# Optimization experiments

Hardware: AMD Instinct MI355X
Metric: run time of the kernel (lower is better)

Reference implementation:

```python
import jax, jax.numpy as jnp
import numpy as np

EMB = 768
HEADS = 12
HEAD_DIM = EMB // HEADS
# Source computes scores / scale with scale = head_dim**-0.5, i.e. scores * sqrt(head_dim)
INV_SCALE = float(HEAD_DIM) ** 0.5


def setup_inputs() -> dict:
    key = jax.random.key(0)
    k1, k2, k3, k4 = jax.random.split(key, 4)
    x = jax.random.normal(k1, (1, 4096, EMB), dtype=jnp.float32)
    qkv_w = jax.random.normal(k2, (3 * EMB, EMB), dtype=jnp.float32) * (EMB ** -0.5)
    out_w = jax.random.normal(k3, (EMB, EMB), dtype=jnp.float32) * (EMB ** -0.5)
    out_b = jax.random.normal(k4, (EMB,), dtype=jnp.float32) * 0.02
    return {"x": x, "qkv_w": qkv_w, "out_w": out_w, "out_b": out_b}


def reference(x, qkv_w, out_w, out_b):
    b, l, d = x.shape
    # qkv: torch Linear (no bias): x @ W^T -> [b, l, 3*d]
    qkv = jnp.einsum('bld,ed->ble', x, qkv_w)
    # rearrange 'b l (n h hd) -> n b h l hd'
    qkv = qkv.reshape(b, l, 3, HEADS, HEAD_DIM).transpose(2, 0, 3, 1, 4)
    q, k, v = qkv[0], qkv[1], qkv[2]
    # scores = (Q K^T) / scale, scale = head_dim**-0.5 => multiply by sqrt(head_dim)
    scores = jnp.einsum('bhqo,bhko->bhqk', q, k) * INV_SCALE
    attn = jax.nn.softmax(scores, axis=-1)  # [b, h, l, l]
    ctx = jnp.einsum('bhqk,bhko->bhqo', attn, v)  # [b, h, l, hd]
    ctx = ctx.transpose(0, 2, 1, 3).reshape(b, l, d)  # 'b h l hd -> b l (h hd)'
    out = jnp.einsum('bld,ed->ble', ctx, out_w) + out_b
    return out
```

## Files before the change

### kernel.cpp

```cpp
#include <hip/hip_runtime.h>

typedef __attribute__((ext_vector_type(8))) short short8;
typedef __attribute__((ext_vector_type(4))) float f32x4;

#define EMB 768
#define SEQ 4096
#define NH 12
#define HD 64
#define QSCALE 11.541560327111707f

#define GLOBAL_AS __attribute__((address_space(1)))
#define LDS_AS __attribute__((address_space(3)))

__device__ inline ushort f2bf(float v) {
  union { float f; unsigned int u; } x; x.f = v;
  unsigned int r = x.u + 0x7fffu + ((x.u >> 16) & 1u);
  return (ushort)(r >> 16);
}
__device__ inline float bf2f(ushort u) {
  union { float f; unsigned int u32; } x; x.u32 = ((unsigned int)u) << 16;
  return x.f;
}

__device__ inline float dpp_max16(float v) {
  int t;
  t = __builtin_amdgcn_update_dpp(0, __float_as_int(v), 0xB1, 0xf, 0xf, true);
  v = fmaxf(v, __int_as_float(t));
  t = __builtin_amdgcn_update_dpp(0, __float_as_int(v), 0x4E, 0xf, 0xf, true);
  v = fmaxf(v, __int_as_float(t));
  t = __builtin_amdgcn_update_dpp(0, __float_as_int(v), 0x124, 0xf, 0xf, true);
  v = fmaxf(v, __int_as_float(t));
  t = __builtin_amdgcn_update_dpp(0, __float_as_int(v), 0x128, 0xf, 0xf, true);
  v = fmaxf(v, __int_as_float(t));
  return v;
}

__global__ void split_all(const float* __restrict__ x, const float* __restrict__ qw,
                          const float* __restrict__ ow,
                          ushort* __restrict__ xh, ushort* __restrict__ xl,
                          ushort* __restrict__ qwh, ushort* __restrict__ qwl,
                          ushort* __restrict__ owh, int n14, int n24) {
  int i = blockIdx.x * blockDim.x + threadIdx.x;
  const float4* src;
  ushort4 *dh, *dl;
  int j;
  if (i < n14) {
    src = (const float4*)x; dh = (ushort4*)xh; dl = (ushort4*)xl; j = i;
  } else if (i < n14 + n24) {
    src = (const float4*)qw; dh = (ushort4*)qwh; dl = (ushort4*)qwl; j = i - n14;
  } else {
    j = i - n14 - n24;
    float4 v = ((const float4*)ow)[j];
    ushort4 h = {f2bf(v.x), f2bf(v.y), f2bf(v.z), f2bf(v.w)};
    ((ushort4*)owh)[j] = h;
    return;
  }
  float4 v = src[j];
  ushort4 h = {f2bf(v.x), f2bf(v.y), f2bf(v.z), f2bf(v.w)};
  ushort4 l = {f2bf(v.x - bf2f(h.x)), f2bf(v.y - bf2f(h.y)),
               f2bf(v.z - bf2f(h.z)), f2bf(v.w - bf2f(h.w))};
  dh[j] = h;
  dl[j] = l;
}

__global__ __launch_bounds__(256, 2) void gemm_bt_split(
    const ushort* __restrict__ Ah, const ushort* __restrict__ Al,
    const ushort* __restrict__ Bh, const ushort* __restrict__ Bl,
    int M, int N, int K, int mode,
    float* __restrict__ Cout, const float* __restrict__ bias,
    ushort* __restrict__ Qh, ushort* __restrict__ Ql,
    ushort* __restrict__ Kh, ushort* __restrict__ Kl,
    ushort* __restrict__ Vt) {
  __shared__ ushort smem[2][4 * 128 * 32];

  const int tid = threadIdx.x;
  const int lane = tid & 63;
  const int w = tid >> 6;
  const int wm = w >> 1, wn = w & 1;
  const int col = lane & 15, quad = lane >> 4;
  const int bm = blockIdx.x, bn = blockIdx.y;

  const bool oneterm = (mode == 2) || (mode == 1 && bn >= 12);
  const bool skipdma = oneterm && (w == 1 || w == 3);

  const ushort* gsrc = (w == 0)   ? Ah + (size_t)bm * 128 * K
                       : (w == 1) ? Al + (size_t)bm * 128 * K
                       : (w == 2) ? Bh + (size_t)bn * 128 * K
                                  : Bl + (size_t)bn * 128 * K;
  const int loff = w * 4096;
  const ushort* g0 = gsrc + (size_t)(lane >> 2) * K + (lane & 3) * 8;

  f32x4 acc[4][4];
  const f32x4 zz = {0.f, 0.f, 0.f, 0.f};
#pragma unroll
  for (int i = 0; i < 4; ++i)
#pragma unroll
    for (int j = 0; j < 4; ++j) acc[i][j] = zz;

#define GSTAGE(b, kt)                                                       \
  if (!skipdma) {                                                           \
    _Pragma("unroll") for (int i = 0; i < 8; ++i) {                         \
      __builtin_amdgcn_global_load_lds(                                     \
          (const GLOBAL_AS unsigned int*)(g0 + (size_t)i * 16 * K + (kt)),  \
          (LDS_AS unsigned int*)(&smem[b][loff + i * 512]), 16, 0, 0);      \
    }                                                                       \
  }

  GSTAGE(0, 0);
  const int nk = K / 32;
  for (int it = 0; it < nk; ++it) {
    const int buf = it & 1;
    asm volatile("s_waitcnt vmcnt(0)" ::: "memory");
    __syncthreads();
    if (it + 1 < nk) GSTAGE(buf ^ 1, (it + 1) * 32);

    const ushort* sAh = &smem[buf][0];
    const ushort* sAl = &smem[buf][4096];
    const ushort* sBh = &smem[buf][8192];
    const ushort* sBl = &smem[buf][12288];

    if (oneterm) {
      short8 fah[4], fbh[4];
#pragma unroll
      for (int t = 0; t < 4; ++t) {
        fah[t] = *(const short8*)(&sAh[(wm * 64 + t * 16 + col) * 32 + quad * 8]);
        fbh[t] = *(const short8*)(&sBh[(wn * 64 + t * 16 + col) * 32 + quad * 8]);
      }
#pragma unroll
      for (int tm = 0; tm < 4; ++tm)
#pragma unroll
        for (int tn = 0; tn < 4; ++tn)
          acc[tm][tn] = __builtin_amdgcn_mfma_f32_16x16x32_bf16(fah[tm], fbh[tn], acc[tm][tn], 0, 0, 0);
    } else {
      short8 fah[4], fal[4], fbh[4], fbl[4];
#pragma unroll
      for (int t = 0; t < 4; ++t) {
        int ra = (wm * 64 + t * 16 + col) * 32 + quad * 8;
        fah[t] = *(const short8*)(&sAh[ra]);
        fal[t] = *(const short8*)(&sAl[ra]);
        int rb = (wn * 64 + t * 16 + col) * 32 + quad * 8;
        fbh[t] = *(const short8*)(&sBh[rb]);
        fbl[t] = *(const short8*)(&sBl[rb]);
      }
#pragma unroll
      for (int tm = 0; tm < 4; ++tm)
#pragma unroll
        for (int tn = 0; tn < 4; ++tn) {
          acc[tm][tn] = __builtin_amdgcn_mfma_f32_16x16x32_bf16(fah[tm], fbh[tn], acc[tm][tn], 0, 0, 0);
          acc[tm][tn] = __builtin_amdgcn_mfma_f32_16x16x32_bf16(fah[tm], fbl[tn], acc[tm][tn], 0, 0, 0);
          acc[tm][tn] = __builtin_amdgcn_mfma_f32_16x16x32_bf16(fal[tm], fbh[tn], acc[tm][tn], 0, 0, 0);
        }
    }
  }

  const int m_base = bm * 128 + wm * 64;
  const int n_base = bn * 128 + wn * 64;

  if (mode != 1) {
#pragma unroll
    for (int tm = 0; tm < 4; ++tm)
#pragma unroll
      for (int tn = 0; tn < 4; ++tn) {
        int gn = n_base + tn * 16 + col;
        float b = bias[gn];
#pragma unroll
        for (int rr = 0; rr < 4; ++rr) {
          int gm = m_base + tm * 16 + quad * 4 + rr;
          Cout[(size_t)gm * N + gn] = acc[tm][tn][rr] + b;
        }
      }
  } else {
    int reg = bn / 6;
    if (reg < 2) {
#pragma unroll
      for (int tm = 0; tm < 4; ++tm)
#pragma unroll
        for (int tn = 0; tn < 4; ++tn) {
          int el = (bn % 6) * 128 + wn * 64 + tn * 16 + col;
          int hh = el >> 6, dd = el & 63;
#pragma unroll
          for (int rr = 0; rr < 4; ++rr) {
            int gm = m_base + tm * 16 + quad * 4 + rr;
            float v = acc[tm][tn][rr];
            if (reg == 0) {
              v *= QSCALE;
              ushort hi = f2bf(v);
              size_t idx = ((size_t)hh * SEQ + gm) * HD + dd;
              Qh[idx] = hi;
              Ql[idx] = f2bf(v - bf2f(hi));
            } else {
              ushort hi = f2bf(v);
              int pc = ((dd >> 3) ^ (gm & 7)) & 7;
              size_t idx = ((size_t)hh * SEQ + gm) * HD + pc * 8 + (dd & 7);
              Kh[idx] = hi;
              Kl[idx] = f2bf(v - bf2f(hi));
            }
          }
        }
    } else {
      __syncthreads();
      ushort* vt_tile = &smem[0][0];
#pragma unroll
      for (int tm = 0; tm < 4; ++tm)
#pragma unroll
        for (int tn = 0; tn < 4; ++tn) {
          int el = wn * 64 + tn * 16 + col;
#pragma unroll
          for (int rr = 0; rr < 4; ++rr) {
            int seq = wm * 64 + tm * 16 + quad * 4 + rr;
            int cc = (((seq >> 3) & 7) ^ (el & 7)) & 7;
            vt_tile[el * 128 + (seq & 64) + cc * 8 + (seq & 7)] = f2bf(acc[tm][tn][rr]);
          }
        }
      __syncthreads();
      int el = tid >> 1;
      int elg = (bn % 6) * 128 + el;
      int hh = elg >> 6, dd = elg & 63;
      ushort* grow = Vt + (size_t)(hh * HD + dd) * SEQ + bm * 128;
#pragma unroll
      for (int i = 0; i < 8; ++i) {
        int c = ((tid & 1) * 8 + i + el) & 15;
        *(uint4*)(grow + c * 8) = *(const uint4*)(&vt_tile[el * 128 + c * 8]);
      }
    }
  }
}

__global__ __launch_bounds__(256, 3) void attn_k(
    const ushort* __restrict__ Qh, const ushort* __restrict__ Ql,
    const ushort* __restrict__ Kh, const ushort* __restrict__ Kl,
    const ushort* __restrict__ Vt, ushort* __restrict__ Ch) {
  __shared__ ushort sKh[2][64 * 64];
  __shared__ ushort sKl[2][64 * 64];
  __shared__ ushort sVt[2][64 * 64];
  __shared__ ushort sP[4][16 * 32];

  const int tid = threadIdx.x, lane = tid & 63, w = tid >> 6;
  const int col = lane & 15, quad = lane >> 4;
  const int h = blockIdx.y;
  const int q0 = blockIdx.x * 64 + w * 16;

  const ushort* qh_base = Qh + ((size_t)h * SEQ + q0 + col) * HD;
  const ushort* ql_base = Ql + ((size_t)h * SEQ + q0 + col) * HD;
  short8 fqh[2], fql[2];
#pragma unroll
  for (int ks = 0; ks < 2; ++ks) {
    fqh[ks] = *(const short8*)(qh_base + ks * 32 + quad * 8);
    fql[ks] = *(const short8*)(ql_base + ks * 32 + quad * 8);
  }

  const short ONE = (short)0x3F80;
  const short8 ones = {ONE, ONE, ONE, ONE, ONE, ONE, ONE, ONE};

  float m2[4], ell[4];
  f32x4 o[4];
  const f32x4 zz = {0.f, 0.f, 0.f, 0.f};
#pragma unroll
  for (int i = 0; i < 4; ++i) { m2[i] = -1e30f; ell[i] = 0.f; o[i] = zz; }

  const ushort* khg = Kh + (size_t)h * SEQ * HD;
  const ushort* klg = Kl + (size_t)h * SEQ * HD;
  const ushort* vtg = Vt + (size_t)h * HD * SEQ;
  ushort* pw = &sP[w][0];

  const ushort* gp[6];
  ushort* lp[6];
  int gstep[6];
#pragma unroll
  for (int i = 0; i < 6; ++i) {
    int idx = w * 6 + i;
    int arr = idx >> 3, j = idx & 7;
    if (arr == 0) {
      gp[i] = khg + (size_t)(j * 8 + (lane >> 3)) * 64 + (lane & 7) * 8;
      lp[i] = &sKh[0][j * 512];
      gstep[i] = 64 * 64;
    } else if (arr == 1) {
      gp[i] = klg + (size_t)(j * 8 + (lane >> 3)) * 64 + (lane & 7) * 8;
      lp[i] = &sKl[0][j * 512];
      gstep[i] = 64 * 64;
    } else {
      gp[i] = vtg + (size_t)(j * 8 + (lane >> 3)) * SEQ + (lane & 7) * 8;
      lp[i] = &sVt[0][j * 512];
      gstep[i] = 64;
    }
  }

#pragma unroll
  for (int i = 0; i < 6; ++i) {
    __builtin_amdgcn_global_load_lds((const GLOBAL_AS unsigned int*)gp[i],
                                     (LDS_AS unsigned int*)lp[i], 16, 0, 0);
    gp[i] += gstep[i];
  }

  const int koff0 = (col * 64 + ((quad ^ (col & 7)) & 7) * 8) * 2;
  const int koff1 = (col * 64 + (((4 + quad) ^ (col & 7)) & 7) * 8) * 2;
  const int fpoff = (col * 32 + ((quad ^ (col & 3) ^ ((col >> 2) & 3)) & 3) * 8) * 2;
  const int voff0 = koff0;
  const int voff1 = koff1;

  auto do_iter = [&](int buf) {
    asm volatile("s_waitcnt vmcnt(0)" ::: "memory");
    __syncthreads();
#pragma unroll
    for (int i = 0; i < 6; ++i) {
      __builtin_amdgcn_global_load_lds(
          (const GLOBAL_AS unsigned int*)gp[i],
          (LDS_AS unsigned int*)(lp[i] + (buf ^ 1) * 4096), 16, 0, 0);
      gp[i] += gstep[i];
    }
    const char* kh = (const char*)&sKh[buf][0];
    const char* kl = (const char*)&sKl[buf][0];
    const char* vt = (const char*)&sVt[buf][0];

    f32x4 s[4];
#pragma unroll
    for (int tn = 0; tn < 4; ++tn) {
      f32x4 a = zz;
      short8 kh0 = *(const short8*)(kh + tn * 2048 + koff0);
      short8 kl0 = *(const short8*)(kl + tn * 2048 + koff0);
      short8 kh1 = *(const short8*)(kh + tn * 2048 + koff1);
      short8 kl1 = *(const short8*)(kl + tn * 2048 + koff1);
      a = __builtin_amdgcn_mfma_f32_16x16x32_bf16(fqh[0], kh0, a, 0, 0, 0);
      a = __builtin_amdgcn_mfma_f32_16x16x32_bf16(fqh[0], kl0, a, 0, 0, 0);
      a = __builtin_amdgcn_mfma_f32_16x16x32_bf16(fql[0], kh0, a, 0, 0, 0);
      a = __builtin_amdgcn_mfma_f32_16x16x32_bf16(fqh[1], kh1, a, 0, 0, 0);
      a = __builtin_amdgcn_mfma_f32_16x16x32_bf16(fqh[1], kl1, a, 0, 0, 0);
      a = __builtin_amdgcn_mfma_f32_16x16x32_bf16(fql[1], kh1, a, 0, 0, 0);
      s[tn] = a;
    }

    float lm[4];
#pragma unroll
    for (int rr = 0; rr < 4; ++rr)
      lm[rr] = fmaxf(fmaxf(s[0][rr], s[1][rr]), fmaxf(s[2][rr], s[3][rr]));
    int cond = (lm[0] <= m2[0]) && (lm[1] <= m2[1]) &&
               (lm[2] <= m2[2]) && (lm[3] <= m2[3]);
    if (!__all(cond)) {
      float alpha[4];
#pragma unroll
      for (int rr = 0; rr < 4; ++rr) {
        float vm = dpp_max16(lm[rr]);
        float mn = fmaxf(m2[rr], vm + 48.0f);
        alpha[rr] = exp2f(m2[rr] - mn);
        m2[rr] = mn;
        ell[rr] *= alpha[rr];
      }
#pragma unroll
      for (int td = 0; td < 4; ++td)
#pragma unroll
        for (int rr = 0; rr < 4; ++rr) o[td][rr] *= alpha[rr];
    }

    f32x4 psum = zz;
#pragma unroll
    for (int hh = 0; hh < 2; ++hh) {
#pragma unroll
      for (int t2 = 0; t2 < 2; ++t2) {
        int tn = hh * 2 + t2;
#pragma unroll
        for (int rr = 0; rr < 4; ++rr) {
          float p = exp2f(s[tn][rr] - m2[rr]);
          int row = quad * 4 + rr;
          int cc = t2 * 16 + col;
          int slot = ((cc >> 3) ^ rr ^ quad) & 3;
          pw[row * 32 + slot * 8 + (cc & 7)] =
              (ushort)(__float_as_uint(p) >> 16);
        }
      }
      asm volatile("s_waitcnt lgkmcnt(0)" ::: "memory");
      short8 fp = *(const short8*)((const char*)pw + fpoff);
      psum = __builtin_amdgcn_mfma_f32_16x16x32_bf16(fp, ones, psum, 0, 0, 0);
      const int vo = hh ? voff1 : voff0;
#pragma unroll
      for (int td = 0; td < 4; ++td) {
        short8 fv = *(const short8*)(vt + td * 2048 + vo);
        o[td] = __builtin_amdgcn_mfma_f32_16x16x32_bf16(fp, fv, o[td], 0, 0, 0);
      }
    }
#pragma unroll
    for (int rr = 0; rr < 4; ++rr) ell[rr] += psum[rr];
  };

  for (int kb = 0; kb < SEQ; kb += 128) {
    do_iter(0);
    do_iter(1);
  }

#pragma unroll
  for (int td = 0; td < 4; ++td)
#pragma unroll
    for (int rr = 0; rr < 4; ++rr) {
      float v = o[td][rr] / ell[rr];
      int l = q0 + quad * 4 + rr;
      int d = h * 64 + td * 16 + col;
      Ch[(size_t)l * EMB + d] = f2bf(v);
    }
}

extern "C" void kernel_launch(void* const* d_in, const int* in_sizes, int n_in,
                              void* d_out, int out_size, void* d_ws, size_t ws_size,
                              hipStream_t stream) {
  const float* x = (const float*)d_in[0];
  const float* qkv_w = (const float*)d_in[1];
  const float* out_w = (const float*)d_in[2];
  const float* out_b = (const float*)d_in[3];
  float* out = (float*)d_out;

  char* p = (char*)d_ws;
  auto carve = [&](size_t bytes) {
    char* q = p;
    p += (bytes + 255) & ~(size_t)255;
    return q;
  };
  const size_t NX = (size_t)SEQ * EMB;
  const size_t NQW = (size_t)3 * EMB * EMB;
  const size_t NOW = (size_t)EMB * EMB;
  const size_t NQKV = (size_t)NH * SEQ * HD;

  ushort* xh = (ushort*)carve(NX * 2);
  ushort* xl = (ushort*)carve(NX * 2);
  ushort* qwh = (ushort*)carve(NQW * 2);
  ushort* qwl = (ushort*)carve(NQW * 2);
  ushort* owh = (ushort*)carve(NOW * 2);
  ushort* Qh = (ushort*)carve(NQKV * 2);
  ushort* Ql = (ushort*)carve(NQKV * 2);
  ushort* Kh = (ushort*)carve(NQKV * 2);
  ushort* Kl = (ushort*)carve(NQKV * 2);
  ushort* Vt = (ushort*)carve(NQKV * 2);
  ushort* Ch = (ushort*)carve(NX * 2);

  const int ntot4 = (int)((NX + NQW + NOW) / 4);
  split_all<<<dim3(ntot4 / 256), 256, 0, stream>>>(
      x, qkv_w, out_w, xh, xl, qwh, qwl, owh, (int)(NX / 4), (int)(NQW / 4));

  gemm_bt_split<<<dim3(32, 18), 256, 0, stream>>>(
      xh, xl, qwh, qwl, SEQ, 3 * EMB, EMB, 1,
      nullptr, nullptr, Qh, Ql, Kh, Kl, Vt);

  attn_k<<<dim3(SEQ / 64, NH), 256, 0, stream>>>(Qh, Ql, Kh, Kl, Vt, Ch);

  gemm_bt_split<<<dim3(32, 6), 256, 0, stream>>>(
      Ch, Ch, owh, owh, SEQ, EMB, EMB, 2,
      out, out_b, nullptr, nullptr, nullptr, nullptr, nullptr);
}
```

Measured before the change: 215.9 us.

## Rewrite attention inner loop with 32x32 MFMA and register-resident P

Switches the attention kernel from 16x16x32 MFMA tiles to 32x32x16 tiles. It computes the transposed S = K·Q^T so the probabilities stay in registers: they are packed with v_cvt_pk_bf16 and permlane32_swap and fed straight to the PV MFMA, which removes the LDS round trip for P. The key dimension of each block is split across two wave pairs, each keeping its own running max and sum, and the two halves are merged through LDS at the end. The aim is fewer LDS accesses, fewer instructions per MFMA, and no ones-MFMA for the row sum. The cost is a final cross-wave reduction and more registers per wave from the 16-wide accumulators.

Result: faster. 202.0 us (-6.4%).

```diff
diff --git a/kernel.cpp b/kernel.cpp
--- a/kernel.cpp
+++ b/kernel.cpp
@@ -2,6 +2,8 @@
 
 typedef __attribute__((ext_vector_type(8))) short short8;
 typedef __attribute__((ext_vector_type(4))) float f32x4;
+typedef __attribute__((ext_vector_type(16))) float f32x16;
+typedef __attribute__((ext_vector_type(2))) unsigned int uint2v;
 
 #define EMB 768
 #define SEQ 4096
@@ -22,17 +24,15 @@
   return x.f;
 }
 
-__device__ inline float dpp_max16(float v) {
-  int t;
-  t = __builtin_amdgcn_update_dpp(0, __float_as_int(v), 0xB1, 0xf, 0xf, true);
-  v = fmaxf(v, __int_as_float(t));
-  t = __builtin_amdgcn_update_dpp(0, __float_as_int(v), 0x4E, 0xf, 0xf, true);
-  v = fmaxf(v, __int_as_float(t));
-  t = __builtin_amdgcn_update_dpp(0, __float_as_int(v), 0x124, 0xf, 0xf, true);
-  v = fmaxf(v, __int_as_float(t));
-  t = __builtin_amdgcn_update_dpp(0, __float_as_int(v), 0x128, 0xf, 0xf, true);
-  v = fmaxf(v, __int_as_float(t));
-  return v;
+__device__ inline int cvt_pk_bf16(float a, float b) {
+  int r;
+  asm("v_cvt_pk_bf16_f32 %0, %1, %2" : "=v"(r) : "v"(a), "v"(b));
+  return r;
+}
+__device__ inline void pswap(int& a, int& b) {
+  uint2v r = __builtin_amdgcn_permlane32_swap((unsigned)a, (unsigned)b, false, false);
+  a = (int)r.x;
+  b = (int)r.y;
 }
 
 __global__ void split_all(const float* __restrict__ x, const float* __restrict__ qw,
@@ -230,39 +230,26 @@
     const ushort* __restrict__ Qh, const ushort* __restrict__ Ql,
     const ushort* __restrict__ Kh, const ushort* __restrict__ Kl,
     const ushort* __restrict__ Vt, ushort* __restrict__ Ch) {
-  __shared__ ushort sKh[2][64 * 64];
-  __shared__ ushort sKl[2][64 * 64];
-  __shared__ ushort sVt[2][64 * 64];
-  __shared__ ushort sP[4][16 * 32];
+  __shared__ __attribute__((aligned(128))) ushort smem[6 * 4096];
 
   const int tid = threadIdx.x, lane = tid & 63, w = tid >> 6;
-  const int col = lane & 15, quad = lane >> 4;
-  const int h = blockIdx.y;
-  const int q0 = blockIdx.x * 64 + w * 16;
-
-  const ushort* qh_base = Qh + ((size_t)h * SEQ + q0 + col) * HD;
-  const ushort* ql_base = Ql + ((size_t)h * SEQ + q0 + col) * HD;
-  short8 fqh[2], fql[2];
-#pragma unroll
-  for (int ks = 0; ks < 2; ++ks) {
-    fqh[ks] = *(const short8*)(qh_base + ks * 32 + quad * 8);
-    fql[ks] = *(const short8*)(ql_base + ks * 32 + quad * 8);
-  }
-
-  const short ONE = (short)0x3F80;
-  const short8 ones = {ONE, ONE, ONE, ONE, ONE, ONE, ONE, ONE};
-
-  float m2[4], ell[4];
-  f32x4 o[4];
-  const f32x4 zz = {0.f, 0.f, 0.f, 0.f};
-#pragma unroll
-  for (int i = 0; i < 4; ++i) { m2[i] = -1e30f; ell[i] = 0.f; o[i] = zz; }
-
-  const ushort* khg = Kh + (size_t)h * SEQ * HD;
-  const ushort* klg = Kl + (size_t)h * SEQ * HD;
-  const ushort* vtg = Vt + (size_t)h * HD * SEQ;
-  ushort* pw = &sP[w][0];
-
+  const int wq = w >> 1, wk = w & 1;
+  const int qc = lane & 31, hl = lane >> 5;
+  const int head = blockIdx.y;
+  const int qb = blockIdx.x * 64 + wq * 32;
+
+  const ushort* qh_base = Qh + ((size_t)head * SEQ + qb + qc) * HD + hl * 8;
+  const ushort* ql_base = Ql + ((size_t)head * SEQ + qb + qc) * HD + hl * 8;
+  short8 fqh[4], fql[4];
+#pragma unroll
+  for (int d = 0; d < 4; ++d) {
+    fqh[d] = *(const short8*)(qh_base + d * 16);
+    fql[d] = *(const short8*)(ql_base + d * 16);
+  }
+
+  const ushort* khg = Kh + (size_t)head * SEQ * HD;
+  const ushort* klg = Kl + (size_t)head * SEQ * HD;
+  const ushort* vtg = Vt + (size_t)head * HD * SEQ;
   const ushort* gp[6];
   ushort* lp[6];
   int gstep[6];
@@ -272,19 +259,18 @@
     int arr = idx >> 3, j = idx & 7;
     if (arr == 0) {
       gp[i] = khg + (size_t)(j * 8 + (lane >> 3)) * 64 + (lane & 7) * 8;
-      lp[i] = &sKh[0][j * 512];
+      lp[i] = &smem[0 + j * 512];
       gstep[i] = 64 * 64;
     } else if (arr == 1) {
       gp[i] = klg + (size_t)(j * 8 + (lane >> 3)) * 64 + (lane & 7) * 8;
-      lp[i] = &sKl[0][j * 512];
+      lp[i] = &smem[8192 + j * 512];
       gstep[i] = 64 * 64;
     } else {
       gp[i] = vtg + (size_t)(j * 8 + (lane >> 3)) * SEQ + (lane & 7) * 8;
-      lp[i] = &sVt[0][j * 512];
+      lp[i] = &smem[16384 + j * 512];
       gstep[i] = 64;
     }
   }
-
 #pragma unroll
   for (int i = 0; i < 6; ++i) {
     __builtin_amdgcn_global_load_lds((const GLOBAL_AS unsigned int*)gp[i],
@@ -292,11 +278,22 @@
     gp[i] += gstep[i];
   }
 
-  const int koff0 = (col * 64 + ((quad ^ (col & 7)) & 7) * 8) * 2;
-  const int koff1 = (col * 64 + (((4 + quad) ^ (col & 7)) & 7) * 8) * 2;
-  const int fpoff = (col * 32 + ((quad ^ (col & 3) ^ ((col >> 2) & 3)) & 3) * 8) * 2;
-  const int voff0 = koff0;
-  const int voff1 = koff1;
+  int koff[4];
+#pragma unroll
+  for (int d = 0; d < 4; ++d)
+    koff[d] = ((wk * 32 + qc) * 64 + (((d * 2 + hl) ^ (qc & 7)) & 7) * 8) * 2;
+  int voff[2][2];
+#pragma unroll
+  for (int td = 0; td < 2; ++td)
+#pragma unroll
+    for (int ks = 0; ks < 2; ++ks)
+      voff[td][ks] =
+          ((td * 32 + qc) * 64 + (((wk * 4 + ks * 2 + hl) ^ (qc & 7)) & 7) * 8) * 2;
+
+  float m2 = -1e30f, ell = 0.f;
+  f32x16 o0, o1;
+#pragma unroll
+  for (int r = 0; r < 16; ++r) { o0[r] = 0.f; o1[r] = 0.f; }
 
   auto do_iter = [&](int buf) {
     asm volatile("s_waitcnt vmcnt(0)" ::: "memory");
@@ -308,77 +305,62 @@
           (LDS_AS unsigned int*)(lp[i] + (buf ^ 1) * 4096), 16, 0, 0);
       gp[i] += gstep[i];
     }
-    const char* kh = (const char*)&sKh[buf][0];
-    const char* kl = (const char*)&sKl[buf][0];
-    const char* vt = (const char*)&sVt[buf][0];
-
-    f32x4 s[4];
-#pragma unroll
-    for (int tn = 0; tn < 4; ++tn) {
-      f32x4 a = zz;
-      short8 kh0 = *(const short8*)(kh + tn * 2048 + koff0);
-      short8 kl0 = *(const short8*)(kl + tn * 2048 + koff0);
-      short8 kh1 = *(const short8*)(kh + tn * 2048 + koff1);
-      short8 kl1 = *(const short8*)(kl + tn * 2048 + koff1);
-      a = __builtin_amdgcn_mfma_f32_16x16x32_bf16(fqh[0], kh0, a, 0, 0, 0);
-      a = __builtin_amdgcn_mfma_f32_16x16x32_bf16(fqh[0], kl0, a, 0, 0, 0);
-      a = __builtin_amdgcn_mfma_f32_16x16x32_bf16(fql[0], kh0, a, 0, 0, 0);
-      a = __builtin_amdgcn_mfma_f32_16x16x32_bf16(fqh[1], kh1, a, 0, 0, 0);
-      a = __builtin_amdgcn_mfma_f32_16x16x32_bf16(fqh[1], kl1, a, 0, 0, 0);
-      a = __builtin_amdgcn_mfma_f32_16x16x32_bf16(fql[1], kh1, a, 0, 0, 0);
-      s[tn] = a;
-    }
-
-    float lm[4];
-#pragma unroll
-    for (int rr = 0; rr < 4; ++rr)
-      lm[rr] = fmaxf(fmaxf(s[0][rr], s[1][rr]), fmaxf(s[2][rr], s[3][rr]));
-    int cond = (lm[0] <= m2[0]) && (lm[1] <= m2[1]) &&
-               (lm[2] <= m2[2]) && (lm[3] <= m2[3]);
-    if (!__all(cond)) {
-      float alpha[4];
-#pragma unroll
-      for (int rr = 0; rr < 4; ++rr) {
-        float vm = dpp_max16(lm[rr]);
-        float mn = fmaxf(m2[rr], vm + 48.0f);
-        alpha[rr] = exp2f(m2[rr] - mn);
-        m2[rr] = mn;
-        ell[rr] *= alpha[rr];
-      }
-#pragma unroll
-      for (int td = 0; td < 4; ++td)
-#pragma unroll
-        for (int rr = 0; rr < 4; ++rr) o[td][rr] *= alpha[rr];
-    }
-
-    f32x4 psum = zz;
-#pragma unroll
-    for (int hh = 0; hh < 2; ++hh) {
-#pragma unroll
-      for (int t2 = 0; t2 < 2; ++t2) {
-        int tn = hh * 2 + t2;
-#pragma unroll
-        for (int rr = 0; rr < 4; ++rr) {
-          float p = exp2f(s[tn][rr] - m2[rr]);
-          int row = quad * 4 + rr;
-          int cc = t2 * 16 + col;
-          int slot = ((cc >> 3) ^ rr ^ quad) & 3;
-          pw[row * 32 + slot * 8 + (cc & 7)] =
-              (ushort)(__float_as_uint(p) >> 16);
-        }
-      }
-      asm volatile("s_waitcnt lgkmcnt(0)" ::: "memory");
-      short8 fp = *(const short8*)((const char*)pw + fpoff);
-      psum = __builtin_amdgcn_mfma_f32_16x16x32_bf16(fp, ones, psum, 0, 0, 0);
-      const int vo = hh ? voff1 : voff0;
-#pragma unroll
-      for (int td = 0; td < 4; ++td) {
-        short8 fv = *(const short8*)(vt + td * 2048 + vo);
-        o[td] = __builtin_amdgcn_mfma_f32_16x16x32_bf16(fp, fv, o[td], 0, 0, 0);
-      }
-    }
-#pragma unroll
-    for (int rr = 0; rr < 4; ++rr) ell[rr] += psum[rr];
+    const char* kh = (const char*)&smem[buf * 4096];
+    const char* kl = (const char*)&smem[8192 + buf * 4096];
+    const char* vt = (const char*)&smem[16384 + buf * 4096];
+
+    f32x16 s;
+#pragma unroll
+    for (int r = 0; r < 16; ++r) s[r] = 0.f;
+#pragma unroll
+    for (int d = 0; d < 4; ++d) {
+      short8 akh = *(const short8*)(kh + koff[d]);
+      short8 akl = *(const short8*)(kl + koff[d]);
+      s = __builtin_amdgcn_mfma_f32_32x32x16_bf16(akh, fqh[d], s, 0, 0, 0);
+      s = __builtin_amdgcn_mfma_f32_32x32x16_bf16(akl, fqh[d], s, 0, 0, 0);
+      s = __builtin_amdgcn_mfma_f32_32x32x16_bf16(akh, fql[d], s, 0, 0, 0);
+    }
+    short8 fv00 = *(const short8*)(vt + voff[0][0]);
+    short8 fv01 = *(const short8*)(vt + voff[0][1]);
+    short8 fv10 = *(const short8*)(vt + voff[1][0]);
+    short8 fv11 = *(const short8*)(vt + voff[1][1]);
+
+    float lm = fmaxf(
+        fmaxf(fmaxf(fmaxf(s[0], s[1]), fmaxf(s[2], s[3])),
+              fmaxf(fmaxf(s[4], s[5]), fmaxf(s[6], s[7]))),
+        fmaxf(fmaxf(fmaxf(s[8], s[9]), fmaxf(s[10], s[11])),
+              fmaxf(fmaxf(s[12], s[13]), fmaxf(s[14], s[15]))));
+    if (!__all(lm <= m2)) {
+      float om = __shfl_xor(lm, 32);
+      float vm = fmaxf(lm, om);
+      float mn = fmaxf(m2, vm + 48.0f);
+      float alpha = exp2f(m2 - mn);
+      m2 = mn;
+      ell *= alpha;
+#pragma unroll
+      for (int r = 0; r < 16; ++r) { o0[r] *= alpha; o1[r] *= alpha; }
+    }
+#pragma unroll
+    for (int r = 0; r < 16; ++r) s[r] = exp2f(s[r] - m2);
+    float ps = (((s[0] + s[1]) + (s[2] + s[3])) + ((s[4] + s[5]) + (s[6] + s[7]))) +
+               (((s[8] + s[9]) + (s[10] + s[11])) + ((s[12] + s[13]) + (s[14] + s[15])));
+    ell += ps;
+
+    int pk[8];
+#pragma unroll
+    for (int d = 0; d < 8; ++d) pk[d] = cvt_pk_bf16(s[2 * d], s[2 * d + 1]);
+    pswap(pk[0], pk[2]);
+    pswap(pk[1], pk[3]);
+    pswap(pk[4], pk[6]);
+    pswap(pk[5], pk[7]);
+    union { int i[4]; short8 s8; } b0, b1;
+    b0.i[0] = pk[0]; b0.i[1] = pk[1]; b0.i[2] = pk[2]; b0.i[3] = pk[3];
+    b1.i[0] = pk[4]; b1.i[1] = pk[5]; b1.i[2] = pk[6]; b1.i[3] = pk[7];
+
+    o0 = __builtin_amdgcn_mfma_f32_32x32x16_bf16(fv00, b0.s8, o0, 0, 0, 0);
+    o0 = __builtin_amdgcn_mfma_f32_32x32x16_bf16(fv01, b1.s8, o0, 0, 0, 0);
+    o1 = __builtin_amdgcn_mfma_f32_32x32x16_bf16(fv10, b0.s8, o1, 0, 0, 0);
+    o1 = __builtin_amdgcn_mfma_f32_32x32x16_bf16(fv11, b1.s8, o1, 0, 0, 0);
   };
 
   for (int kb = 0; kb < SEQ; kb += 128) {
@@ -386,15 +368,38 @@
     do_iter(1);
   }
 
-#pragma unroll
-  for (int td = 0; td < 4; ++td)
-#pragma unroll
-    for (int rr = 0; rr < 4; ++rr) {
-      float v = o[td][rr] / ell[rr];
-      int l = q0 + quad * 4 + rr;
-      int d = h * 64 + td * 16 + col;
-      Ch[(size_t)l * EMB + d] = f2bf(v);
-    }
+  ell += __shfl_xor(ell, 32);
+
+  __syncthreads();
+  float* ob = (float*)&smem[4096 + wq * 8192];
+  float* mel = (float*)&smem[20480];
+  if (wk == 1) {
+    *(f32x16*)(ob + lane * 32) = o0;
+    *(f32x16*)(ob + lane * 32 + 16) = o1;
+    mel[wq * 128 + lane] = m2;
+    mel[wq * 128 + 64 + lane] = ell;
+  }
+  __syncthreads();
+  if (wk == 0) {
+    float m2B = mel[wq * 128 + lane];
+    float ellB = mel[wq * 128 + 64 + lane];
+    f32x16 p0 = *(const f32x16*)(ob + lane * 32);
+    f32x16 p1 = *(const f32x16*)(ob + lane * 32 + 16);
+    float mN = fmaxf(m2, m2B);
+    float aA = exp2f(m2 - mN), aB = exp2f(m2B - mN);
+    float inv = 1.0f / (ell * aA + ellB * aB);
+    ushort* crow = Ch + (size_t)(qb + qc) * EMB + head * 64 + hl * 4;
+#pragma unroll
+    for (int r = 0; r < 8; ++r) {
+      int off = ((2 * r) & 3) + 8 * (r >> 1);
+      float v0 = (o0[2 * r] * aA + p0[2 * r] * aB) * inv;
+      float v1 = (o0[2 * r + 1] * aA + p0[2 * r + 1] * aB) * inv;
+      *(unsigned int*)(crow + off) = (unsigned int)cvt_pk_bf16(v0, v1);
+      float w0 = (o1[2 * r] * aA + p1[2 * r] * aB) * inv;
+      float w1 = (o1[2 * r + 1] * aA + p1[2 * r + 1] * aB) * inv;
+      *(unsigned int*)(crow + 32 + off) = (unsigned int)cvt_pk_bf16(w0, w1);
+    }
+  }
 }
 
 extern "C" void kernel_launch(void* const* d_in, const int* in_sizes, int n_in,
```
